# Optimization experiments

Hardware: AMD Instinct MI355X
Metric: run time of the kernel (lower is better)

## Reference

```python
import jax, jax.numpy as jnp
import numpy as np

B, N, D = 256, 400, 512
K = 20  # args.gcn_topk == self.k


def setup_inputs() -> dict:
    key = jax.random.key(0)
    k1, k2, k3, k4 = jax.random.split(key, 4)
    node_embs = jax.random.normal(k1, (B, N, D), dtype=jnp.float32)
    h_t = jax.random.normal(k2, (B, D), dtype=jnp.float32)
    mask = jnp.ones((B, N), dtype=jnp.float32)  # unused by forward, kept for signature fidelity
    # mapper = Linear(rnn_dim=512, gcn_dim=512) followed by Tanh
    lim = 1.0 / np.sqrt(D)
    W_map = jax.random.uniform(k3, (D, D), dtype=jnp.float32, minval=-lim, maxval=lim)
    b_map = jax.random.uniform(k4, (D,), dtype=jnp.float32, minval=-lim, maxval=lim)
    return {"node_embs": node_embs, "mask": mask, "h_t": h_t, "W_map": W_map, "b_map": b_map}


def reference(node_embs, mask, h_t, W_map, b_map):
    # scorer = Tanh(Linear(h_t.detach()))  -> [B, D]
    scorer = jnp.tanh(jax.lax.stop_gradient(h_t) @ W_map.T + b_map)
    # scores = bmm(node_embs, scorer) / ||scorer||  -> [B, N]
    scores = jnp.einsum('bnd,bd->bn', node_embs, scorer)
    scores = scores / jnp.linalg.norm(scorer, axis=1, keepdims=True)
    # top-k over nodes
    vals, topk_indices = jax.lax.top_k(scores, K)  # [B, K]
    # vals are always finite => topk_indices_out == topk_indices;
    # repeat_num = K/K + 1 = 2, then truncated back to K => no-op
    topk_indices_out = topk_indices
    # gather rows topk_indices; the original expand(-1,-1,gcn_topk) selects only
    # the FIRST K feature columns -> out is [B, K, K]
    gathered = jnp.take_along_axis(node_embs[:, :, :K], topk_indices[:, :, None], axis=1)
    tanh_s = jnp.tanh(jnp.take_along_axis(scores, topk_indices, axis=1))  # [B, K]
    out = gathered * tanh_s[:, :, None]  # [B, K, K]
    # softmax over nodes, entropy of the categorical, log-prob gather
    logp = jax.nn.log_softmax(scores, axis=1)  # [B, N]
    probs = jnp.exp(logp)
    entropy_object = -jnp.sum(probs * logp, axis=1)  # [B]
    score = jnp.take_along_axis(logp, topk_indices, axis=-1)  # [B, K]
    policy_score = jnp.mean(score, axis=1)  # [B]
    return (jnp.swapaxes(out, 1, 2), policy_score, scorer, entropy_object, topk_indices_out)
```

## Files before the change

### kernel.cpp

```cpp
#include <hip/hip_runtime.h>
#include <math.h>
#include <float.h>

#define BB 256
#define NN 400
#define DD 512
#define KK 20

__device__ __forceinline__ float dot8(float4 a0, float4 a1, float4 b0, float4 b1) {
    return a0.x*b0.x + a0.y*b0.y + a0.z*b0.z + a0.w*b0.w
         + a1.x*b1.x + a1.y*b1.y + a1.z*b1.z + a1.w*b1.w;
}

__global__ __launch_bounds__(1024, 4) void fused_topk_kernel(
    const float* __restrict__ embs,
    const float* __restrict__ h_t,
    const float* __restrict__ W,
    const float* __restrict__ bmap,
    float* __restrict__ out0,
    float* __restrict__ out1,
    float* __restrict__ out2,
    float* __restrict__ out3,
    float* __restrict__ out4)
{
    const int b = blockIdx.x;
    const int t = threadIdx.x;
    const int wave = t >> 6, lane = t & 63;

    __shared__ float sh_sc[DD];
    __shared__ float sh_s[NN];
    __shared__ float redf[16], redf2[16], redq[8];
    __shared__ float mZ[3];
    __shared__ int   sh_topk[KK];
    __shared__ float sh_th[KK];

    const float4* hp = (const float4*)(h_t + (size_t)b * DD);
    const float4 h0 = hp[lane];
    const float4 h1 = hp[lane + 64];

    {
        const int d0 = wave * 32;
        #pragma unroll 4
        for (int p = 0; p < 16; ++p) {
            const int d = d0 + p * 2;
            const float4* wp0 = (const float4*)(W + (size_t)d * DD);
            const float4* wp1 = (const float4*)(W + (size_t)(d + 1) * DD);
            float4 a0 = wp0[lane], a1 = wp0[lane + 64];
            float4 c0 = wp1[lane], c1 = wp1[lane + 64];
            float s0 = dot8(a0, a1, h0, h1);
            float s1 = dot8(c0, c1, h0, h1);
            #pragma unroll
            for (int off = 32; off; off >>= 1) {
                s0 += __shfl_xor(s0, off, 64);
                s1 += __shfl_xor(s1, off, 64);
            }
            if (lane == 0) {
                sh_sc[d]     = tanhf(s0 + bmap[d]);
                sh_sc[d + 1] = tanhf(s1 + bmap[d + 1]);
            }
        }
    }
    __syncthreads();

    if (t < DD) out2[(size_t)b * DD + t] = sh_sc[t];
    if (wave < 8) {
        float v = sh_sc[t];
        float ss = v * v;
        #pragma unroll
        for (int off = 32; off; off >>= 1) ss += __shfl_xor(ss, off, 64);
        if (lane == 0) redq[wave] = ss;
    }

    const float4 g0 = ((const float4*)sh_sc)[lane];
    const float4 g1 = ((const float4*)sh_sc)[lane + 64];
    {
        const int n0 = wave * 25;
        const float* base = embs + ((size_t)b * NN + n0) * DD;
        #pragma unroll 4
        for (int p = 0; p < 12; ++p) {
            const float4* p0 = (const float4*)(base + (size_t)(2 * p) * DD);
            const float4* p1 = (const float4*)(base + (size_t)(2 * p + 1) * DD);
            float4 a0 = p0[lane], a1 = p0[lane + 64];
            float4 c0 = p1[lane], c1 = p1[lane + 64];
            float s0 = dot8(a0, a1, g0, g1);
            float s1 = dot8(c0, c1, g0, g1);
            #pragma unroll
            for (int off = 32; off; off >>= 1) {
                s0 += __shfl_xor(s0, off, 64);
                s1 += __shfl_xor(s1, off, 64);
            }
            if (lane == 0) {
                sh_s[n0 + 2 * p]     = s0;
                sh_s[n0 + 2 * p + 1] = s1;
            }
        }
        {
            const float4* p0 = (const float4*)(base + (size_t)24 * DD);
            float4 a0 = p0[lane], a1 = p0[lane + 64];
            float s0 = dot8(a0, a1, g0, g1);
            #pragma unroll
            for (int off = 32; off; off >>= 1) s0 += __shfl_xor(s0, off, 64);
            if (lane == 0) sh_s[n0 + 24] = s0;
        }
    }
    __syncthreads();

    if (t == 0) {
        float tot = 0.f;
        #pragma unroll
        for (int i = 0; i < 8; ++i) tot += redq[i];
        mZ[0] = 1.0f / sqrtf(tot);
    }
    __syncthreads();
    const float inv = mZ[0];

    const float x = (t < NN) ? sh_s[t] * inv : -FLT_MAX;
    {
        float m = x;
        #pragma unroll
        for (int off = 32; off; off >>= 1) m = fmaxf(m, __shfl_xor(m, off, 64));
        if (lane == 0) redf[wave] = m;
    }
    __syncthreads();
    if (t == 0) {
        float m = redf[0];
        #pragma unroll
        for (int i = 1; i < 16; ++i) m = fmaxf(m, redf[i]);
        mZ[1] = m;
    }
    __syncthreads();
    const float m = mZ[1];

    {
        float e = 0.f, wv = 0.f;
        if (t < NN) {
            float d = x - m;
            e = expf(d);
            wv = e * d;
        }
        #pragma unroll
        for (int off = 32; off; off >>= 1) {
            e  += __shfl_xor(e, off, 64);
            wv += __shfl_xor(wv, off, 64);
        }
        if (lane == 0) { redf[wave] = e; redf2[wave] = wv; }
    }
    __syncthreads();
    if (t == 0) {
        float Z = 0.f, Ws = 0.f;
        #pragma unroll
        for (int i = 0; i < 16; ++i) { Z += redf[i]; Ws += redf2[i]; }
        float logZ = logf(Z);
        mZ[2] = logZ;
        out3[b] = logZ - Ws / Z;
    }
    __syncthreads();
    const float logZ = mZ[2];

    if (wave == 0) {
        float v0 = sh_s[lane      ] * inv;
        float v1 = sh_s[lane +  64] * inv;
        float v2 = sh_s[lane + 128] * inv;
        float v3 = sh_s[lane + 192] * inv;
        float v4 = sh_s[lane + 256] * inv;
        float v5 = sh_s[lane + 320] * inv;
        float v6 = (lane + 384 < NN) ? sh_s[lane + 384] * inv : -FLT_MAX;
        float acc = 0.f;
        for (int k = 0; k < KK; ++k) {
            float bv = v0; int bi = lane;
            if (v1 > bv) { bv = v1; bi = lane + 64; }
            if (v2 > bv) { bv = v2; bi = lane + 128; }
            if (v3 > bv) { bv = v3; bi = lane + 192; }
            if (v4 > bv) { bv = v4; bi = lane + 256; }
            if (v5 > bv) { bv = v5; bi = lane + 320; }
            if (v6 > bv) { bv = v6; bi = lane + 384; }
            #pragma unroll
            for (int off = 32; off; off >>= 1) {
                float ov = __shfl_xor(bv, off, 64);
                int   oi = __shfl_xor(bi, off, 64);
                if (ov > bv || (ov == bv && oi < bi)) { bv = ov; bi = oi; }
            }
            if (lane == 0) {
                sh_topk[k] = bi;
                sh_th[k] = tanhf(bv);
                out4[(size_t)b * KK + k] = (float)bi;
                acc += bv - m - logZ;
            }
            v0 = (bi == lane      ) ? -FLT_MAX : v0;
            v1 = (bi == lane +  64) ? -FLT_MAX : v1;
            v2 = (bi == lane + 128) ? -FLT_MAX : v2;
            v3 = (bi == lane + 192) ? -FLT_MAX : v3;
            v4 = (bi == lane + 256) ? -FLT_MAX : v4;
            v5 = (bi == lane + 320) ? -FLT_MAX : v5;
            v6 = (bi == lane + 384) ? -FLT_MAX : v6;
        }
        if (lane == 0) out1[b] = acc / (float)KK;
    }
    __syncthreads();

    if (t < NN) {
        int k = t / KK;
        int j = t - k * KK;
        float val = embs[((size_t)b * NN + sh_topk[k]) * DD + j] * sh_th[k];
        out0[(size_t)b * (KK * KK) + j * KK + k] = val;
    }
}

extern "C" void kernel_launch(void* const* d_in, const int* in_sizes, int n_in,
                              void* d_out, int out_size, void* d_ws, size_t ws_size,
                              hipStream_t stream) {
    const float* node_embs = (const float*)d_in[0];
    const float* h_t   = (const float*)d_in[2];
    const float* W_map = (const float*)d_in[3];
    const float* b_map = (const float*)d_in[4];

    float* ob = (float*)d_out;
    float* out0 = ob;
    float* out1 = ob + 102400;
    float* out2 = ob + 102656;
    float* out3 = ob + 233728;
    float* out4 = ob + 233984;

    fused_topk_kernel<<<BB, 1024, 0, stream>>>(node_embs, h_t, W_map, b_map,
                                               out0, out1, out2, out3, out4);
}
```

Before: 66.35 us.

## Split scorer GEMV into separate kernel and defer score reductions via shared partials

Moves the tanh(h_t W^T + b) scorer computation into its own kernel, where each block keeps W rows in registers and reuses them across 32 batches, instead of every batch block re-reading the full 1 MB W matrix. The main kernel reads the precomputed scorer from the output buffer. Its node-score loop now issues 5 rows of loads at once and writes per-lane partial dot products to a padded shared array, with one thread per node summing them, which removes the per-row wave shuffle reductions. The cost is an extra kernel launch with a dependency between the two kernels, plus about 100 KB of shared memory per block, which may reduce occupancy.

```diff
diff --git a/kernel.cpp b/kernel.cpp
--- a/kernel.cpp
+++ b/kernel.cpp
@@ -12,14 +12,48 @@
          + a1.x*b1.x + a1.y*b1.y + a1.z*b1.z + a1.w*b1.w;
 }
 
-__global__ __launch_bounds__(1024, 4) void fused_topk_kernel(
-    const float* __restrict__ embs,
+__global__ __launch_bounds__(1024) void scorer_kernel(
     const float* __restrict__ h_t,
     const float* __restrict__ W,
     const float* __restrict__ bmap,
+    float* __restrict__ out2)
+{
+    const int blk = blockIdx.x;
+    const int dc = blk & 15, bg = blk >> 4;
+    const int wave = threadIdx.x >> 6, lane = threadIdx.x & 63;
+
+    const int d0 = dc * 32 + wave * 2;
+    const int d1 = d0 + 1;
+    const float4* wp0 = (const float4*)(W + (size_t)d0 * DD);
+    const float4* wp1 = (const float4*)(W + (size_t)d1 * DD);
+    const float4 w00 = wp0[lane], w01 = wp0[lane + 64];
+    const float4 w10 = wp1[lane], w11 = wp1[lane + 64];
+    const float bias0 = bmap[d0], bias1 = bmap[d1];
+
+    #pragma unroll 4
+    for (int bi = 0; bi < 32; ++bi) {
+        const int b = bg * 32 + bi;
+        const float4* hp = (const float4*)(h_t + (size_t)b * DD);
+        float4 hb0 = hp[lane], hb1 = hp[lane + 64];
+        float p0 = dot8(w00, w01, hb0, hb1);
+        float p1 = dot8(w10, w11, hb0, hb1);
+        #pragma unroll
+        for (int off = 32; off; off >>= 1) {
+            p0 += __shfl_xor(p0, off, 64);
+            p1 += __shfl_xor(p1, off, 64);
+        }
+        if (lane == 0) {
+            out2[(size_t)b * DD + d0] = tanhf(p0 + bias0);
+            out2[(size_t)b * DD + d1] = tanhf(p1 + bias1);
+        }
+    }
+}
+
+__global__ __launch_bounds__(1024, 4) void fused_topk_kernel(
+    const float* __restrict__ embs,
+    const float* __restrict__ scorer,
     float* __restrict__ out0,
     float* __restrict__ out1,
-    float* __restrict__ out2,
     float* __restrict__ out3,
     float* __restrict__ out4)
 {
@@ -27,6 +61,7 @@
     const int t = threadIdx.x;
     const int wave = t >> 6, lane = t & 63;
 
+    __shared__ float part[NN][65];
     __shared__ float sh_sc[DD];
     __shared__ float sh_s[NN];
     __shared__ float redf[16], redf2[16], redq[8];
@@ -34,73 +69,33 @@
     __shared__ int   sh_topk[KK];
     __shared__ float sh_th[KK];
 
-    const float4* hp = (const float4*)(h_t + (size_t)b * DD);
-    const float4 h0 = hp[lane];
-    const float4 h1 = hp[lane + 64];
-
-    {
-        const int d0 = wave * 32;
-        #pragma unroll 4
-        for (int p = 0; p < 16; ++p) {
-            const int d = d0 + p * 2;
-            const float4* wp0 = (const float4*)(W + (size_t)d * DD);
-            const float4* wp1 = (const float4*)(W + (size_t)(d + 1) * DD);
-            float4 a0 = wp0[lane], a1 = wp0[lane + 64];
-            float4 c0 = wp1[lane], c1 = wp1[lane + 64];
-            float s0 = dot8(a0, a1, h0, h1);
-            float s1 = dot8(c0, c1, h0, h1);
-            #pragma unroll
-            for (int off = 32; off; off >>= 1) {
-                s0 += __shfl_xor(s0, off, 64);
-                s1 += __shfl_xor(s1, off, 64);
-            }
-            if (lane == 0) {
-                sh_sc[d]     = tanhf(s0 + bmap[d]);
-                sh_sc[d + 1] = tanhf(s1 + bmap[d + 1]);
-            }
-        }
-    }
-    __syncthreads();
-
-    if (t < DD) out2[(size_t)b * DD + t] = sh_sc[t];
-    if (wave < 8) {
-        float v = sh_sc[t];
+    if (t < DD) {
+        float v = scorer[(size_t)b * DD + t];
+        sh_sc[t] = v;
         float ss = v * v;
         #pragma unroll
         for (int off = 32; off; off >>= 1) ss += __shfl_xor(ss, off, 64);
         if (lane == 0) redq[wave] = ss;
     }
+    __syncthreads();
 
     const float4 g0 = ((const float4*)sh_sc)[lane];
     const float4 g1 = ((const float4*)sh_sc)[lane + 64];
+
     {
         const int n0 = wave * 25;
-        const float* base = embs + ((size_t)b * NN + n0) * DD;
-        #pragma unroll 4
-        for (int p = 0; p < 12; ++p) {
-            const float4* p0 = (const float4*)(base + (size_t)(2 * p) * DD);
-            const float4* p1 = (const float4*)(base + (size_t)(2 * p + 1) * DD);
-            float4 a0 = p0[lane], a1 = p0[lane + 64];
-            float4 c0 = p1[lane], c1 = p1[lane + 64];
-            float s0 = dot8(a0, a1, g0, g1);
-            float s1 = dot8(c0, c1, g0, g1);
+        const float* rowbase = embs + ((size_t)b * NN + n0) * DD;
+        for (int g = 0; g < 5; ++g) {
+            float4 A0[5], A1[5];
             #pragma unroll
-            for (int off = 32; off; off >>= 1) {
-                s0 += __shfl_xor(s0, off, 64);
-                s1 += __shfl_xor(s1, off, 64);
+            for (int r = 0; r < 5; ++r) {
+                const float4* p = (const float4*)(rowbase + (size_t)(g * 5 + r) * DD);
+                A0[r] = p[lane];
+                A1[r] = p[lane + 64];
             }
-            if (lane == 0) {
-                sh_s[n0 + 2 * p]     = s0;
-                sh_s[n0 + 2 * p + 1] = s1;
-            }
-        }
-        {
-            const float4* p0 = (const float4*)(base + (size_t)24 * DD);
-            float4 a0 = p0[lane], a1 = p0[lane + 64];
-            float s0 = dot8(a0, a1, g0, g1);
             #pragma unroll
-            for (int off = 32; off; off >>= 1) s0 += __shfl_xor(s0, off, 64);
-            if (lane == 0) sh_s[n0 + 24] = s0;
+            for (int r = 0; r < 5; ++r)
+                part[n0 + g * 5 + r][lane] = dot8(A0[r], A1[r], g0, g1);
         }
     }
     __syncthreads();
@@ -111,10 +106,22 @@
         for (int i = 0; i < 8; ++i) tot += redq[i];
         mZ[0] = 1.0f / sqrtf(tot);
     }
+
+    float raw = 0.f;
+    if (t < NN) {
+        const float* pr = part[t];
+        float a0 = 0.f, a1 = 0.f, a2 = 0.f, a3 = 0.f;
+        #pragma unroll
+        for (int i = 0; i < 64; i += 4) {
+            a0 += pr[i]; a1 += pr[i + 1]; a2 += pr[i + 2]; a3 += pr[i + 3];
+        }
+        raw = (a0 + a1) + (a2 + a3);
+        sh_s[t] = raw;
+    }
     __syncthreads();
     const float inv = mZ[0];
 
-    const float x = (t < NN) ? sh_s[t] * inv : -FLT_MAX;
+    const float x = (t < NN) ? raw * inv : -FLT_MAX;
     {
         float m = x;
         #pragma unroll
@@ -213,6 +220,7 @@
     const float* h_t   = (const float*)d_in[2];
     const float* W_map = (const float*)d_in[3];
     const float* b_map = (const float*)d_in[4];
+    (void)d_ws; (void)ws_size; (void)in_sizes; (void)n_in; (void)out_size;
 
     float* ob = (float*)d_out;
     float* out0 = ob;
@@ -221,6 +229,6 @@
     float* out3 = ob + 233728;
     float* out4 = ob + 233984;
 
-    fused_topk_kernel<<<BB, 1024, 0, stream>>>(node_embs, h_t, W_map, b_map,
-                                               out0, out1, out2, out3, out4);
-}
+    scorer_kernel<<<128, 1024, 0, stream>>>(h_t, W_map, b_map, out2);
+    fused_topk_kernel<<<BB, 1024, 0, stream>>>(node_embs, out2, out0, out1, out3, out4);
+}
```

New measurement: 74.26 us. +11.9%, slower.

## Split each batch row across four blocks with last-block-done atomic reduction

Applied to the files above, without the earlier changes.

The kernel now launches four 256-thread blocks per batch row instead of one 1024-thread block. Each block computes a 128-wide slice of the scorer and partial node scores over that D-chunk, and writes them to workspace. An atomic counter picks the last-arriving block, which sums the partials and runs the softmax, entropy, top-k and gather. This is meant to spread the memory-bound embedding read over more blocks and CUs. In exchange it adds a memset launch, workspace traffic, threadfences, and an atomic serialization per row.

```diff
diff --git a/kernel.cpp b/kernel.cpp
--- a/kernel.cpp
+++ b/kernel.cpp
@@ -6,13 +6,15 @@
 #define NN 400
 #define DD 512
 #define KK 20
+#define NCH 4
+#define CHD 128
 
 __device__ __forceinline__ float dot8(float4 a0, float4 a1, float4 b0, float4 b1) {
     return a0.x*b0.x + a0.y*b0.y + a0.z*b0.z + a0.w*b0.w
          + a1.x*b1.x + a1.y*b1.y + a1.z*b1.z + a1.w*b1.w;
 }
 
-__global__ __launch_bounds__(1024, 4) void fused_topk_kernel(
+__global__ __launch_bounds__(256, 4) void fused_all_kernel(
     const float* __restrict__ embs,
     const float* __restrict__ h_t,
     const float* __restrict__ W,
@@ -21,135 +23,151 @@
     float* __restrict__ out1,
     float* __restrict__ out2,
     float* __restrict__ out3,
-    float* __restrict__ out4)
+    float* __restrict__ out4,
+    float* __restrict__ ws_partial,
+    float* __restrict__ ws_ss,
+    int*   __restrict__ ws_cnt)
 {
-    const int b = blockIdx.x;
+    const int blk = blockIdx.x;
+    const int b = blk >> 2, c = blk & 3;
     const int t = threadIdx.x;
     const int wave = t >> 6, lane = t & 63;
 
-    __shared__ float sh_sc[DD];
+    __shared__ float sc_lds[CHD];
+    __shared__ float red[4], red2[4];
     __shared__ float sh_s[NN];
-    __shared__ float redf[16], redf2[16], redq[8];
     __shared__ float mZ[3];
     __shared__ int   sh_topk[KK];
     __shared__ float sh_th[KK];
+    __shared__ int   sh_flag;
 
     const float4* hp = (const float4*)(h_t + (size_t)b * DD);
-    const float4 h0 = hp[lane];
-    const float4 h1 = hp[lane + 64];
-
-    {
-        const int d0 = wave * 32;
+    const float4 h0 = hp[lane], h1 = hp[lane + 64];
+    {
+        const int dbase = c * CHD + wave * 32;
         #pragma unroll 4
         for (int p = 0; p < 16; ++p) {
-            const int d = d0 + p * 2;
-            const float4* wp0 = (const float4*)(W + (size_t)d * DD);
-            const float4* wp1 = (const float4*)(W + (size_t)(d + 1) * DD);
+            const int d0 = dbase + 2 * p, d1 = d0 + 1;
+            const float4* wp0 = (const float4*)(W + (size_t)d0 * DD);
+            const float4* wp1 = (const float4*)(W + (size_t)d1 * DD);
             float4 a0 = wp0[lane], a1 = wp0[lane + 64];
-            float4 c0 = wp1[lane], c1 = wp1[lane + 64];
-            float s0 = dot8(a0, a1, h0, h1);
-            float s1 = dot8(c0, c1, h0, h1);
+            float4 b0 = wp1[lane], b1 = wp1[lane + 64];
+            float p0 = dot8(a0, a1, h0, h1);
+            float p1 = dot8(b0, b1, h0, h1);
             #pragma unroll
             for (int off = 32; off; off >>= 1) {
-                s0 += __shfl_xor(s0, off, 64);
-                s1 += __shfl_xor(s1, off, 64);
+                p0 += __shfl_xor(p0, off, 64);
+                p1 += __shfl_xor(p1, off, 64);
             }
             if (lane == 0) {
-                sh_sc[d]     = tanhf(s0 + bmap[d]);
-                sh_sc[d + 1] = tanhf(s1 + bmap[d + 1]);
-            }
-        }
-    }
-    __syncthreads();
-
-    if (t < DD) out2[(size_t)b * DD + t] = sh_sc[t];
-    if (wave < 8) {
-        float v = sh_sc[t];
+                sc_lds[d0 - c * CHD] = tanhf(p0 + bmap[d0]);
+                sc_lds[d1 - c * CHD] = tanhf(p1 + bmap[d1]);
+            }
+        }
+    }
+    __syncthreads();
+
+    if (t < CHD) {
+        float v = sc_lds[t];
+        out2[(size_t)b * DD + c * CHD + t] = v;
         float ss = v * v;
         #pragma unroll
         for (int off = 32; off; off >>= 1) ss += __shfl_xor(ss, off, 64);
-        if (lane == 0) redq[wave] = ss;
-    }
-
-    const float4 g0 = ((const float4*)sh_sc)[lane];
-    const float4 g1 = ((const float4*)sh_sc)[lane + 64];
-    {
-        const int n0 = wave * 25;
-        const float* base = embs + ((size_t)b * NN + n0) * DD;
-        #pragma unroll 4
-        for (int p = 0; p < 12; ++p) {
-            const float4* p0 = (const float4*)(base + (size_t)(2 * p) * DD);
-            const float4* p1 = (const float4*)(base + (size_t)(2 * p + 1) * DD);
-            float4 a0 = p0[lane], a1 = p0[lane + 64];
-            float4 c0 = p1[lane], c1 = p1[lane + 64];
-            float s0 = dot8(a0, a1, g0, g1);
-            float s1 = dot8(c0, c1, g0, g1);
-            #pragma unroll
-            for (int off = 32; off; off >>= 1) {
-                s0 += __shfl_xor(s0, off, 64);
-                s1 += __shfl_xor(s1, off, 64);
-            }
-            if (lane == 0) {
-                sh_s[n0 + 2 * p]     = s0;
-                sh_s[n0 + 2 * p + 1] = s1;
-            }
-        }
-        {
-            const float4* p0 = (const float4*)(base + (size_t)24 * DD);
-            float4 a0 = p0[lane], a1 = p0[lane + 64];
-            float s0 = dot8(a0, a1, g0, g1);
-            #pragma unroll
-            for (int off = 32; off; off >>= 1) s0 += __shfl_xor(s0, off, 64);
-            if (lane == 0) sh_s[n0 + 24] = s0;
-        }
-    }
-    __syncthreads();
-
+        if (lane == 0) red[wave] = ss;
+    }
+    __syncthreads();
+    if (t == 0) ws_ss[b * NCH + c] = red[0] + red[1];
+
+    {
+        const int half = lane >> 5;
+        const int col  = lane & 31;
+        const float4 sc4 = ((const float4*)sc_lds)[col];
+        const float4* base4 = (const float4*)(embs
+            + ((size_t)b * NN + wave * 100 + half) * DD + c * CHD);
+        float* pout = ws_partial + ((size_t)(b * NCH + c)) * NN + wave * 100;
+
+        for (int g = 0; g < 10; ++g) {
+            float4 A[5];
+            #pragma unroll
+            for (int r = 0; r < 5; ++r)
+                A[r] = base4[col + (size_t)(5 * g + r) * 256];
+            float s[5];
+            #pragma unroll
+            for (int r = 0; r < 5; ++r)
+                s[r] = A[r].x * sc4.x + A[r].y * sc4.y + A[r].z * sc4.z + A[r].w * sc4.w;
+            #pragma unroll
+            for (int off = 1; off < 32; off <<= 1) {
+                #pragma unroll
+                for (int r = 0; r < 5; ++r) s[r] += __shfl_xor(s[r], off, 64);
+            }
+            if (col == 0) {
+                #pragma unroll
+                for (int r = 0; r < 5; ++r) pout[2 * (5 * g + r) + half] = s[r];
+            }
+        }
+    }
+
+    __threadfence();
+    __syncthreads();
     if (t == 0) {
-        float tot = 0.f;
-        #pragma unroll
-        for (int i = 0; i < 8; ++i) tot += redq[i];
+        int old = atomicAdd(ws_cnt + b, 1);
+        sh_flag = (old == NCH - 1) ? 1 : 0;
+    }
+    __syncthreads();
+    if (!sh_flag) return;
+    __threadfence();
+
+    const float* pb = ws_partial + (size_t)b * NCH * NN;
+    float r0 = 0.f, r1 = 0.f;
+    {
+        r0 = pb[t] + pb[NN + t] + pb[2 * NN + t] + pb[3 * NN + t];
+        if (t < NN - 256) {
+            int n = t + 256;
+            r1 = pb[n] + pb[NN + n] + pb[2 * NN + n] + pb[3 * NN + n];
+        }
+    }
+    if (t == 0) {
+        float tot = ws_ss[b * NCH] + ws_ss[b * NCH + 1]
+                  + ws_ss[b * NCH + 2] + ws_ss[b * NCH + 3];
         mZ[0] = 1.0f / sqrtf(tot);
     }
     __syncthreads();
     const float inv = mZ[0];
-
-    const float x = (t < NN) ? sh_s[t] * inv : -FLT_MAX;
-    {
-        float m = x;
+    const float x0 = r0 * inv;
+    const float x1 = (t < NN - 256) ? r1 * inv : -FLT_MAX;
+    sh_s[t] = x0;
+    if (t < NN - 256) sh_s[t + 256] = x1;
+
+    {
+        float m = fmaxf(x0, x1);
         #pragma unroll
         for (int off = 32; off; off >>= 1) m = fmaxf(m, __shfl_xor(m, off, 64));
-        if (lane == 0) redf[wave] = m;
-    }
-    __syncthreads();
-    if (t == 0) {
-        float m = redf[0];
-        #pragma unroll
-        for (int i = 1; i < 16; ++i) m = fmaxf(m, redf[i]);
-        mZ[1] = m;
-    }
+        if (lane == 0) red[wave] = m;
+    }
+    __syncthreads();
+    if (t == 0) mZ[1] = fmaxf(fmaxf(red[0], red[1]), fmaxf(red[2], red[3]));
     __syncthreads();
     const float m = mZ[1];
 
     {
-        float e = 0.f, wv = 0.f;
-        if (t < NN) {
-            float d = x - m;
-            e = expf(d);
-            wv = e * d;
+        float d0 = x0 - m;
+        float e = expf(d0), wv = e * d0;
+        if (t < NN - 256) {
+            float d1 = x1 - m;
+            float e1 = expf(d1);
+            e += e1; wv += e1 * d1;
         }
         #pragma unroll
         for (int off = 32; off; off >>= 1) {
             e  += __shfl_xor(e, off, 64);
             wv += __shfl_xor(wv, off, 64);
         }
-        if (lane == 0) { redf[wave] = e; redf2[wave] = wv; }
+        if (lane == 0) { red[wave] = e; red2[wave] = wv; }
     }
     __syncthreads();
     if (t == 0) {
-        float Z = 0.f, Ws = 0.f;
-        #pragma unroll
-        for (int i = 0; i < 16; ++i) { Z += redf[i]; Ws += redf2[i]; }
+        float Z = red[0] + red[1] + red[2] + red[3];
+        float Ws = red2[0] + red2[1] + red2[2] + red2[3];
         float logZ = logf(Z);
         mZ[2] = logZ;
         out3[b] = logZ - Ws / Z;
@@ -158,13 +176,13 @@
     const float logZ = mZ[2];
 
     if (wave == 0) {
-        float v0 = sh_s[lane      ] * inv;
-        float v1 = sh_s[lane +  64] * inv;
-        float v2 = sh_s[lane + 128] * inv;
-        float v3 = sh_s[lane + 192] * inv;
-        float v4 = sh_s[lane + 256] * inv;
-        float v5 = sh_s[lane + 320] * inv;
-        float v6 = (lane + 384 < NN) ? sh_s[lane + 384] * inv : -FLT_MAX;
+        float v0 = sh_s[lane      ];
+        float v1 = sh_s[lane +  64];
+        float v2 = sh_s[lane + 128];
+        float v3 = sh_s[lane + 192];
+        float v4 = sh_s[lane + 256];
+        float v5 = sh_s[lane + 320];
+        float v6 = (lane + 384 < NN) ? sh_s[lane + 384] : -FLT_MAX;
         float acc = 0.f;
         for (int k = 0; k < KK; ++k) {
             float bv = v0; int bi = lane;
@@ -213,6 +231,7 @@
     const float* h_t   = (const float*)d_in[2];
     const float* W_map = (const float*)d_in[3];
     const float* b_map = (const float*)d_in[4];
+    (void)in_sizes; (void)n_in; (void)out_size; (void)ws_size;
 
     float* ob = (float*)d_out;
     float* out0 = ob;
@@ -221,6 +240,14 @@
     float* out3 = ob + 233728;
     float* out4 = ob + 233984;
 
-    fused_topk_kernel<<<BB, 1024, 0, stream>>>(node_embs, h_t, W_map, b_map,
-                                               out0, out1, out2, out3, out4);
+    int*   ws_cnt     = (int*)d_ws;
+    float* ws_ss      = (float*)d_ws + 256;
+    float* ws_partial = (float*)d_ws + 256 + 1024;
+
+    hipMemsetAsync(ws_cnt, 0, BB * sizeof(int), stream);
+
+    fused_all_kernel<<<BB * NCH, 256, 0, stream>>>(
+        node_embs, h_t, W_map, b_map,
+        out0, out1, out2, out3, out4,
+        ws_partial, ws_ss, ws_cnt);
 }
```

Result: slower. 208.2 us (+213.8%).

## Split each dot product across 8-lane groups so waves process 8 rows at once

Applied to the files above, without the earlier changes.

Both matvecs (the h_t·W mapper and the node_embs·scorer scores) now give each 8-lane group its own row. Each lane keeps 16 float4 chunks of the vector in registers and accumulates over 16 strided loads, then a 3-step shuffle finishes the sum. This replaces the full 64-lane butterfly per row, cutting shuffle and reduction overhead and raising memory-level parallelism per wave. Bias-add and tanh move out of lane 0 into a parallel per-element pass after the first barrier. The cost is higher register use, with 16 float4 per lane, under a 1024-thread block bound.

```diff
diff --git a/kernel.cpp b/kernel.cpp
--- a/kernel.cpp
+++ b/kernel.cpp
@@ -6,11 +6,6 @@
 #define NN 400
 #define DD 512
 #define KK 20
-
-__device__ __forceinline__ float dot8(float4 a0, float4 a1, float4 b0, float4 b1) {
-    return a0.x*b0.x + a0.y*b0.y + a0.z*b0.z + a0.w*b0.w
-         + a1.x*b1.x + a1.y*b1.y + a1.z*b1.z + a1.w*b1.w;
-}
 
 __global__ __launch_bounds__(1024, 4) void fused_topk_kernel(
     const float* __restrict__ embs,
@@ -26,6 +21,8 @@
     const int b = blockIdx.x;
     const int t = threadIdx.x;
     const int wave = t >> 6, lane = t & 63;
+    const int q  = lane & 7;
+    const int rr = lane >> 3;
 
     __shared__ float sh_sc[DD];
     __shared__ float sh_s[NN];
@@ -34,73 +31,89 @@
     __shared__ int   sh_topk[KK];
     __shared__ float sh_th[KK];
 
-    const float4* hp = (const float4*)(h_t + (size_t)b * DD);
-    const float4 h0 = hp[lane];
-    const float4 h1 = hp[lane + 64];
-
-    {
-        const int d0 = wave * 32;
-        #pragma unroll 4
-        for (int p = 0; p < 16; ++p) {
-            const int d = d0 + p * 2;
-            const float4* wp0 = (const float4*)(W + (size_t)d * DD);
-            const float4* wp1 = (const float4*)(W + (size_t)(d + 1) * DD);
-            float4 a0 = wp0[lane], a1 = wp0[lane + 64];
-            float4 c0 = wp1[lane], c1 = wp1[lane + 64];
-            float s0 = dot8(a0, a1, h0, h1);
-            float s1 = dot8(c0, c1, h0, h1);
-            #pragma unroll
-            for (int off = 32; off; off >>= 1) {
-                s0 += __shfl_xor(s0, off, 64);
-                s1 += __shfl_xor(s1, off, 64);
-            }
-            if (lane == 0) {
-                sh_sc[d]     = tanhf(s0 + bmap[d]);
-                sh_sc[d + 1] = tanhf(s1 + bmap[d + 1]);
-            }
-        }
-    }
-    __syncthreads();
-
-    if (t < DD) out2[(size_t)b * DD + t] = sh_sc[t];
-    if (wave < 8) {
-        float v = sh_sc[t];
+    {
+        const float4* hb = (const float4*)(h_t + (size_t)b * DD);
+        float4 S[16];
+        #pragma unroll
+        for (int k = 0; k < 16; ++k) S[k] = hb[q + 8 * k];
+
+        #pragma unroll
+        for (int j = 0; j < 4; ++j) {
+            const int row = (j * 16 + wave) * 8 + rr;
+            const float4* src = (const float4*)(W + (size_t)row * DD) + q;
+            float a0 = 0.f, a1 = 0.f, a2 = 0.f, a3 = 0.f;
+            #pragma unroll
+            for (int k = 0; k < 16; ++k) {
+                float4 e = src[8 * k];
+                a0 += e.x * S[k].x;
+                a1 += e.y * S[k].y;
+                a2 += e.z * S[k].z;
+                a3 += e.w * S[k].w;
+            }
+            float acc = (a0 + a1) + (a2 + a3);
+            acc += __shfl_xor(acc, 1, 64);
+            acc += __shfl_xor(acc, 2, 64);
+            acc += __shfl_xor(acc, 4, 64);
+            if (q == 0) sh_sc[row] = acc;
+        }
+    }
+    __syncthreads();
+
+    if (t < DD) {
+        float v = tanhf(sh_sc[t] + bmap[t]);
+        sh_sc[t] = v;
+        out2[(size_t)b * DD + t] = v;
         float ss = v * v;
         #pragma unroll
         for (int off = 32; off; off >>= 1) ss += __shfl_xor(ss, off, 64);
         if (lane == 0) redq[wave] = ss;
     }
-
-    const float4 g0 = ((const float4*)sh_sc)[lane];
-    const float4 g1 = ((const float4*)sh_sc)[lane + 64];
-    {
-        const int n0 = wave * 25;
-        const float* base = embs + ((size_t)b * NN + n0) * DD;
-        #pragma unroll 4
-        for (int p = 0; p < 12; ++p) {
-            const float4* p0 = (const float4*)(base + (size_t)(2 * p) * DD);
-            const float4* p1 = (const float4*)(base + (size_t)(2 * p + 1) * DD);
-            float4 a0 = p0[lane], a1 = p0[lane + 64];
-            float4 c0 = p1[lane], c1 = p1[lane + 64];
-            float s0 = dot8(a0, a1, g0, g1);
-            float s1 = dot8(c0, c1, g0, g1);
-            #pragma unroll
-            for (int off = 32; off; off >>= 1) {
-                s0 += __shfl_xor(s0, off, 64);
-                s1 += __shfl_xor(s1, off, 64);
-            }
-            if (lane == 0) {
-                sh_s[n0 + 2 * p]     = s0;
-                sh_s[n0 + 2 * p + 1] = s1;
-            }
-        }
-        {
-            const float4* p0 = (const float4*)(base + (size_t)24 * DD);
-            float4 a0 = p0[lane], a1 = p0[lane + 64];
-            float s0 = dot8(a0, a1, g0, g1);
-            #pragma unroll
-            for (int off = 32; off; off >>= 1) s0 += __shfl_xor(s0, off, 64);
-            if (lane == 0) sh_s[n0 + 24] = s0;
+    __syncthreads();
+
+    {
+        const float4* scb = (const float4*)sh_sc;
+        float4 S[16];
+        #pragma unroll
+        for (int k = 0; k < 16; ++k) S[k] = scb[q + 8 * k];
+
+        const float* ebase = embs + (size_t)b * NN * DD;
+
+        #pragma unroll
+        for (int j = 0; j < 3; ++j) {
+            const int row = (j * 16 + wave) * 8 + rr;
+            const float4* src = (const float4*)(ebase + (size_t)row * DD) + q;
+            float a0 = 0.f, a1 = 0.f, a2 = 0.f, a3 = 0.f;
+            #pragma unroll
+            for (int k = 0; k < 16; ++k) {
+                float4 e = src[8 * k];
+                a0 += e.x * S[k].x;
+                a1 += e.y * S[k].y;
+                a2 += e.z * S[k].z;
+                a3 += e.w * S[k].w;
+            }
+            float acc = (a0 + a1) + (a2 + a3);
+            acc += __shfl_xor(acc, 1, 64);
+            acc += __shfl_xor(acc, 2, 64);
+            acc += __shfl_xor(acc, 4, 64);
+            if (q == 0) sh_s[row] = acc;
+        }
+        if (wave < 2) {
+            const int row = (48 + wave) * 8 + rr;
+            const float4* src = (const float4*)(ebase + (size_t)row * DD) + q;
+            float a0 = 0.f, a1 = 0.f, a2 = 0.f, a3 = 0.f;
+            #pragma unroll
+            for (int k = 0; k < 16; ++k) {
+                float4 e = src[8 * k];
+                a0 += e.x * S[k].x;
+                a1 += e.y * S[k].y;
+                a2 += e.z * S[k].z;
+                a3 += e.w * S[k].w;
+            }
+            float acc = (a0 + a1) + (a2 + a3);
+            acc += __shfl_xor(acc, 1, 64);
+            acc += __shfl_xor(acc, 2, 64);
+            acc += __shfl_xor(acc, 4, 64);
+            if (q == 0) sh_s[row] = acc;
         }
     }
     __syncthreads();
@@ -213,6 +226,7 @@
     const float* h_t   = (const float*)d_in[2];
     const float* W_map = (const float*)d_in[3];
     const float* b_map = (const float*)d_in[4];
+    (void)in_sizes; (void)n_in; (void)out_size; (void)d_ws; (void)ws_size;
 
     float* ob = (float*)d_out;
     float* out0 = ob;
@@ -221,6 +235,6 @@
     float* out3 = ob + 233728;
     float* out4 = ob + 233984;
 
-    fused_topk_kernel<<<BB, 1024, 0, stream>>>(node_embs, h_t, W_map, b_map,
-                                               out0, out1, out2, out3, out4);
+    fused_topk_kernel<<<BB, 1024, 0, stream>>>(
+        node_embs, h_t, W_map, b_map, out0, out1, out2, out3, out4);
 }
```

Measured after the change: 67.67 us. About the same (+2.0%).
